# Kernel optimization log

Measured on AMD Instinct MI355X. Metric: run time of the kernel, lower is better.

Reference implementation:

```python
import jax, jax.numpy as jnp
import numpy as np

B, S, H = 32, 2048, 1024

def setup_inputs() -> dict:
    key = jax.random.key(0)
    ks = jax.random.split(key, 8)
    scale = 1.0 / np.sqrt(H)
    return {
        "query": jax.random.normal(ks[0], (B, H), jnp.float32),
        "keys": jax.random.normal(ks[1], (B, S, H), jnp.float32),
        "Wa_w": jax.random.uniform(ks[2], (H, H), jnp.float32, -scale, scale),
        "Wa_b": jax.random.uniform(ks[3], (H,), jnp.float32, -scale, scale),
        "Ua_w": jax.random.uniform(ks[4], (H, H), jnp.float32, -scale, scale),
        "Ua_b": jax.random.uniform(ks[5], (H,), jnp.float32, -scale, scale),
        "Va_w": jax.random.uniform(ks[6], (1, H), jnp.float32, -scale, scale),
        "Va_b": jax.random.uniform(ks[7], (1,), jnp.float32, -scale, scale),
    }

def reference(query, keys, Wa_w, Wa_b, Ua_w, Ua_b, Va_w, Va_b):
    # q_proj: [B, H]; k_proj: [B, S, H]  (torch Linear: x @ W^T + b)
    q_proj = query @ Wa_w.T + Wa_b
    k_proj = jnp.einsum("bsh,gh->bsg", keys, Ua_w) + Ua_b
    # scores: [B, S, 1] via thin Va projection of tanh-combined features
    scores = jnp.tanh(q_proj[:, None, :] + k_proj) @ Va_w.T + Va_b
    weights = jax.nn.softmax(scores, axis=1)            # [B, S, 1]
    context = jnp.einsum("bsx,bsh->bxh", weights, keys)  # [B, 1, H]
    return context, weights[:, :, 0]
```

## Files before the change

kernel.cpp:

```cpp
#include <hip/hip_runtime.h>
#include <hip/hip_bf16.h>
#include <stdint.h>

#define B_ 32
#define S_ 2048
#define H_ 1024

typedef __attribute__((ext_vector_type(8))) short short8;
typedef __attribute__((ext_vector_type(4))) float floatx4;

__device__ inline unsigned short f32_bf16(float f) {
    union { float f; unsigned u; } v; v.f = f;
    unsigned u = v.u;
    u += 0x7fff + ((u >> 16) & 1);
    return (unsigned short)(u >> 16);
}
__device__ inline unsigned pack_bf2(float a, float b) {
    return (unsigned)f32_bf16(a) | ((unsigned)f32_bf16(b) << 16);
}
__device__ inline float bf_lo(unsigned u) { union { unsigned u; float f; } v; v.u = u << 16; return v.f; }
__device__ inline float bf_hi(unsigned u) { union { unsigned u; float f; } v; v.u = u & 0xffff0000u; return v.f; }

__device__ inline float tanh_fast(float x) {
    float e = __expf(2.0f * x);
    return 1.0f - 2.0f / (e + 1.0f);
}

__device__ inline void gld16(const void* g, void* l) {
    __builtin_amdgcn_global_load_lds(
        (const __attribute__((address_space(1))) unsigned int*)g,
        (__attribute__((address_space(3))) unsigned int*)l, 16, 0, 0);
}

#define KCVT_BLOCKS 32768
#define UACVT_BLOCKS 512
#define ZS_BLOCKS 64
__global__ void k_prep(const float* __restrict__ keys, unsigned short* __restrict__ keysbf,
                       const float* __restrict__ ua, unsigned short* __restrict__ uab,
                       float* __restrict__ scores) {
    int blk = blockIdx.x, t = threadIdx.x;
    if (blk < KCVT_BLOCKS + UACVT_BLOCKS) {
        const float* src; unsigned short* dst; size_t base;
        if (blk < KCVT_BLOCKS) { src = keys; dst = keysbf; base = (size_t)blk * 2048; }
        else { src = ua; dst = uab; base = (size_t)(blk - KCVT_BLOCKS) * 2048; }
        float4 v0 = *(const float4*)(src + base + t * 4);
        float4 v1 = *(const float4*)(src + base + 1024 + t * 4);
        *(uint2*)(dst + base + t * 4)        = make_uint2(pack_bf2(v0.x, v0.y), pack_bf2(v0.z, v0.w));
        *(uint2*)(dst + base + 1024 + t * 4) = make_uint2(pack_bf2(v1.x, v1.y), pack_bf2(v1.z, v1.w));
    } else {
        int zb = blk - KCVT_BLOCKS - UACVT_BLOCKS;
        float4 z = {0.f, 0.f, 0.f, 0.f};
        *(float4*)(scores + zb * 1024 + t * 4) = z;
    }
}

__global__ void k_qproj(const float* __restrict__ query, const float* __restrict__ Wa_w,
                        const float* __restrict__ Wa_b, const float* __restrict__ Ua_b,
                        float* __restrict__ qsum) {
    __shared__ float qs_l[32][68];
    int g0 = blockIdx.x * 16;
    int t = threadIdx.x;
    int r = t >> 4;
    int l = t & 15;
    int g = g0 + r;
    float acc[32];
#pragma unroll
    for (int b = 0; b < 32; ++b) acc[b] = 0.0f;

    int sb = t >> 3;
    int sc = (t & 7) * 8;
    for (int hc = 0; hc < 16; ++hc) {
        __syncthreads();
        float4 v0 = *(const float4*)(query + (size_t)sb * H_ + hc * 64 + sc);
        float4 v1 = *(const float4*)(query + (size_t)sb * H_ + hc * 64 + sc + 4);
        *(float4*)&qs_l[sb][sc]     = v0;
        *(float4*)&qs_l[sb][sc + 4] = v1;
        __syncthreads();
        float4 w = *(const float4*)(Wa_w + (size_t)g * H_ + hc * 64 + l * 4);
#pragma unroll
        for (int b = 0; b < 32; ++b) {
            float4 q4 = *(const float4*)&qs_l[b][l * 4];
            acc[b] += w.x * q4.x + w.y * q4.y + w.z * q4.z + w.w * q4.w;
        }
    }
#pragma unroll
    for (int b = 0; b < 32; ++b) {
        float a = acc[b];
        a += __shfl_xor(a, 1); a += __shfl_xor(a, 2);
        a += __shfl_xor(a, 4); a += __shfl_xor(a, 8);
        acc[b] = a;
    }
    if (l == 0) {
        float bias = Wa_b[g] + Ua_b[g];
#pragma unroll
        for (int b = 0; b < 32; ++b) qsum[b * H_ + g] = acc[b] + bias;
    }
}

#define BM 128
#define BN 128
#define BK 32

__global__ __launch_bounds__(256, 3) void k_scores(
    const unsigned short* __restrict__ keysbf, const unsigned short* __restrict__ uab,
    const float* __restrict__ qsum, const float* __restrict__ va,
    float* __restrict__ scores)
{
    __shared__ unsigned short Al[BM * BK];
    __shared__ unsigned short Bl[BN * BK];

    int bx = blockIdx.x;
    int x  = bx & 7;
    int i  = bx >> 3;
    int tile_m = x * 64 + (i >> 3);
    int nc     = i & 7;
    int m_base = tile_m * BM;
    int b      = m_base >> 11;
    int g0     = nc * BN;

    int tid = threadIdx.x;
    int wid = tid >> 6, lane = tid & 63;
    int wm = wid >> 1, wn = wid & 1;
    int q = lane >> 4, cn = lane & 15;

    int rl = lane >> 2, cg = lane & 3;
    int rA0 = wid * 32 + rl,      rA1 = wid * 32 + 16 + rl;
    int gA0 = cg ^ ((rA0 >> 1) & 3), gA1 = cg ^ ((rA1 >> 1) & 3);
    const unsigned short* pA0 = keysbf + (size_t)(m_base + rA0) * H_ + gA0 * 8;
    const unsigned short* pA1 = keysbf + (size_t)(m_base + rA1) * H_ + gA1 * 8;
    const unsigned short* pB0 = uab + (size_t)(g0 + rA0) * H_ + gA0 * 8;
    const unsigned short* pB1 = uab + (size_t)(g0 + rA1) * H_ + gA1 * 8;
    unsigned short* lA0 = &Al[(wid * 32) * BK];
    unsigned short* lA1 = &Al[(wid * 32 + 16) * BK];
    unsigned short* lB0 = &Bl[(wid * 32) * BK];
    unsigned short* lB1 = &Bl[(wid * 32 + 16) * BK];

    int aoff[4], boff[4];
#pragma unroll
    for (int ii = 0; ii < 4; ++ii) {
        int r = wm * 64 + ii * 16 + cn;
        aoff[ii] = r * BK + (q ^ ((r >> 1) & 3)) * 8;
        int rb = wn * 64 + ii * 16 + cn;
        boff[ii] = rb * BK + (q ^ ((rb >> 1) & 3)) * 8;
    }

    floatx4 acc[4][4];
#pragma unroll
    for (int ii = 0; ii < 4; ++ii)
#pragma unroll
        for (int jj = 0; jj < 4; ++jj)
            acc[ii][jj] = (floatx4)(0.0f);

    for (int kc = 0; kc < H_ / BK; ++kc) {
        __syncthreads();
        int ko = kc * BK;
        gld16(pA0 + ko, lA0);
        gld16(pA1 + ko, lA1);
        gld16(pB0 + ko, lB0);
        gld16(pB1 + ko, lB1);
        __syncthreads();
        short8 af[4], bf[4];
#pragma unroll
        for (int ii = 0; ii < 4; ++ii) af[ii] = *(const short8*)&Al[aoff[ii]];
#pragma unroll
        for (int jj = 0; jj < 4; ++jj) bf[jj] = *(const short8*)&Bl[boff[jj]];
#pragma unroll
        for (int ii = 0; ii < 4; ++ii)
#pragma unroll
            for (int jj = 0; jj < 4; ++jj)
                acc[ii][jj] = __builtin_amdgcn_mfma_f32_16x16x32_bf16(
                    af[ii], bf[jj], acc[ii][jj], 0, 0, 0);
    }

    float qs[4], vw[4];
#pragma unroll
    for (int jj = 0; jj < 4; ++jj) {
        int g = g0 + wn * 64 + jj * 16 + cn;
        qs[jj] = qsum[b * H_ + g];
        vw[jj] = va[g];
    }
#pragma unroll
    for (int ii = 0; ii < 4; ++ii) {
        float rs[4] = {0.f, 0.f, 0.f, 0.f};
#pragma unroll
        for (int jj = 0; jj < 4; ++jj) {
#pragma unroll
            for (int r = 0; r < 4; ++r)
                rs[r] += vw[jj] * tanh_fast(qs[jj] + acc[ii][jj][r]);
        }
#pragma unroll
        for (int r = 0; r < 4; ++r) {
            for (int mm = 1; mm < 16; mm <<= 1)
                rs[r] += __shfl_xor(rs[r], mm);
        }
        if (cn == 0) {
            int msrow = m_base + wm * 64 + ii * 16 + q * 4;
            float* sp = scores + b * S_ + (msrow & (S_ - 1));
            atomicAdd(sp + 0, rs[0]);
            atomicAdd(sp + 1, rs[1]);
            atomicAdd(sp + 2, rs[2]);
            atomicAdd(sp + 3, rs[3]);
        }
    }
}

__global__ void k_softmax(const float* __restrict__ scores, float* __restrict__ weights) {
    int b = blockIdx.x;
    int t = threadIdx.x;
    __shared__ float red[4];
    float v[8];
    float mx = -1e30f;
#pragma unroll
    for (int k = 0; k < 8; ++k) { v[k] = scores[b * S_ + t + k * 256]; mx = fmaxf(mx, v[k]); }
    for (int mm = 1; mm < 64; mm <<= 1) mx = fmaxf(mx, __shfl_xor(mx, mm));
    if ((t & 63) == 0) red[t >> 6] = mx;
    __syncthreads();
    mx = fmaxf(fmaxf(red[0], red[1]), fmaxf(red[2], red[3]));
    float sum = 0.0f;
#pragma unroll
    for (int k = 0; k < 8; ++k) { v[k] = __expf(v[k] - mx); sum += v[k]; }
    for (int mm = 1; mm < 64; mm <<= 1) sum += __shfl_xor(sum, mm);
    __syncthreads();
    if ((t & 63) == 0) red[t >> 6] = sum;
    __syncthreads();
    sum = red[0] + red[1] + red[2] + red[3];
    float inv = 1.0f / sum;
#pragma unroll
    for (int k = 0; k < 8; ++k) weights[b * S_ + t + k * 256] = v[k] * inv;
}

__global__ void k_ctx1(const unsigned short* __restrict__ keysbf,
                       const float* __restrict__ weights, float* __restrict__ partial) {
    int blk = blockIdx.x;
    int b = blk >> 5, sc = blk & 31;
    int t = threadIdx.x;
    __shared__ float wl[64];
    if (t < 64) wl[t] = weights[b * S_ + sc * 64 + t];
    __syncthreads();
    const uint4* kp = (const uint4*)(keysbf + (size_t)(b * S_ + sc * 64) * H_);
    int col = t & 127;
    int rp  = t >> 7;
    float a0=0,a1=0,a2=0,a3=0,a4=0,a5=0,a6=0,a7=0;
#pragma unroll 8
    for (int s = rp; s < 64; s += 2) {
        uint4 v = kp[(size_t)s * 128 + col];
        float w = wl[s];
        a0 += w * bf_lo(v.x); a1 += w * bf_hi(v.x);
        a2 += w * bf_lo(v.y); a3 += w * bf_hi(v.y);
        a4 += w * bf_lo(v.z); a5 += w * bf_hi(v.z);
        a6 += w * bf_lo(v.w); a7 += w * bf_hi(v.w);
    }
    float* pp = partial + (size_t)(b * 64 + sc * 2 + rp) * H_ + col * 8;
    float4 o0 = {a0, a1, a2, a3}, o1 = {a4, a5, a6, a7};
    *(float4*)pp = o0;
    *(float4*)(pp + 4) = o1;
}

__global__ void k_ctx2(const float* __restrict__ partial, float* __restrict__ ctx) {
    int b = blockIdx.x;
    int t = threadIdx.x;
    float4 a = {0.f, 0.f, 0.f, 0.f};
#pragma unroll 8
    for (int j = 0; j < 64; ++j) {
        float4 p = *(const float4*)(partial + (size_t)(b * 64 + j) * H_ + t * 4);
        a.x += p.x; a.y += p.y; a.z += p.z; a.w += p.w;
    }
    *(float4*)(ctx + b * H_ + t * 4) = a;
}

extern "C" void kernel_launch(void* const* d_in, const int* in_sizes, int n_in,
                              void* d_out, int out_size, void* d_ws, size_t ws_size,
                              hipStream_t stream) {
    const float* query = (const float*)d_in[0];
    const float* keys  = (const float*)d_in[1];
    const float* Wa_w  = (const float*)d_in[2];
    const float* Wa_b  = (const float*)d_in[3];
    const float* Ua_w  = (const float*)d_in[4];
    const float* Ua_b  = (const float*)d_in[5];
    const float* Va_w  = (const float*)d_in[6];

    float* out     = (float*)d_out;
    float* ctx     = out;
    float* weights = out + B_ * H_;

    char* ws = (char*)d_ws;
    unsigned short* keysbf = (unsigned short*)ws;
    unsigned short* uab    = (unsigned short*)(ws + 134217728);
    float*          qsum   = (float*)(ws + 134217728 + 2097152);
    float*          scores = (float*)(ws + 134217728 + 2097152 + 131072);
    float*          partial= (float*)(ws + 134217728 + 2097152 + 131072 + 262144);

    k_prep   <<<KCVT_BLOCKS + UACVT_BLOCKS + ZS_BLOCKS, 256, 0, stream>>>(keys, keysbf, Ua_w, uab, scores);
    k_qproj  <<<64, 256, 0, stream>>>(query, Wa_w, Wa_b, Ua_b, qsum);
    k_scores <<<4096, 256, 0, stream>>>(keysbf, uab, qsum, Va_w, scores);
    k_softmax<<<B_, 256, 0, stream>>>(scores, weights);
    k_ctx1   <<<B_ * 32, 256, 0, stream>>>(keysbf, weights, partial);
    k_ctx2   <<<B_, 256, 0, stream>>>(partial, ctx);
}
```

Before: 627.7 us.

## Double GEMM K-tile to 64 with 8-way swizzle and fold qproj into prep kernel

The scores GEMM now stages a 64-wide K slice per iteration instead of 32, with a new XOR swizzle over 8 column groups and two MFMA sub-steps per tile. This halves the number of barrier-separated load/compute iterations and the synchronisation overhead. The query projection is merged into the prep kernel as extra blocks, removing one kernel launch and letting it overlap with the conversion work. LDS use per block doubles to 32KB, which may reduce occupancy at the requested 3 blocks per CU. The prep kernel also now carries the qproj shared array and register load.

```diff
diff --git a/kernel.cpp b/kernel.cpp
--- a/kernel.cpp
+++ b/kernel.cpp
@@ -35,9 +35,13 @@
 #define KCVT_BLOCKS 32768
 #define UACVT_BLOCKS 512
 #define ZS_BLOCKS 64
+#define QP_BLOCKS 64
 __global__ void k_prep(const float* __restrict__ keys, unsigned short* __restrict__ keysbf,
                        const float* __restrict__ ua, unsigned short* __restrict__ uab,
-                       float* __restrict__ scores) {
+                       float* __restrict__ scores,
+                       const float* __restrict__ query, const float* __restrict__ Wa_w,
+                       const float* __restrict__ Wa_b, const float* __restrict__ Ua_b,
+                       float* __restrict__ qsum) {
     int blk = blockIdx.x, t = threadIdx.x;
     if (blk < KCVT_BLOCKS + UACVT_BLOCKS) {
         const float* src; unsigned short* dst; size_t base;
@@ -47,59 +51,51 @@
         float4 v1 = *(const float4*)(src + base + 1024 + t * 4);
         *(uint2*)(dst + base + t * 4)        = make_uint2(pack_bf2(v0.x, v0.y), pack_bf2(v0.z, v0.w));
         *(uint2*)(dst + base + 1024 + t * 4) = make_uint2(pack_bf2(v1.x, v1.y), pack_bf2(v1.z, v1.w));
-    } else {
+    } else if (blk < KCVT_BLOCKS + UACVT_BLOCKS + ZS_BLOCKS) {
         int zb = blk - KCVT_BLOCKS - UACVT_BLOCKS;
         float4 z = {0.f, 0.f, 0.f, 0.f};
         *(float4*)(scores + zb * 1024 + t * 4) = z;
-    }
-}
-
-__global__ void k_qproj(const float* __restrict__ query, const float* __restrict__ Wa_w,
-                        const float* __restrict__ Wa_b, const float* __restrict__ Ua_b,
-                        float* __restrict__ qsum) {
-    __shared__ float qs_l[32][68];
-    int g0 = blockIdx.x * 16;
-    int t = threadIdx.x;
-    int r = t >> 4;
-    int l = t & 15;
-    int g = g0 + r;
-    float acc[32];
-#pragma unroll
-    for (int b = 0; b < 32; ++b) acc[b] = 0.0f;
-
-    int sb = t >> 3;
-    int sc = (t & 7) * 8;
-    for (int hc = 0; hc < 16; ++hc) {
-        __syncthreads();
-        float4 v0 = *(const float4*)(query + (size_t)sb * H_ + hc * 64 + sc);
-        float4 v1 = *(const float4*)(query + (size_t)sb * H_ + hc * 64 + sc + 4);
-        *(float4*)&qs_l[sb][sc]     = v0;
-        *(float4*)&qs_l[sb][sc + 4] = v1;
-        __syncthreads();
-        float4 w = *(const float4*)(Wa_w + (size_t)g * H_ + hc * 64 + l * 4);
+    } else {
+        __shared__ float qs_l[32][68];
+        int g0 = (blk - KCVT_BLOCKS - UACVT_BLOCKS - ZS_BLOCKS) * 16;
+        int r = t >> 4, l = t & 15;
+        int g = g0 + r;
+        float acc[32];
+#pragma unroll
+        for (int b = 0; b < 32; ++b) acc[b] = 0.0f;
+        int sb = t >> 3, sc = (t & 7) * 8;
+        for (int hc = 0; hc < 16; ++hc) {
+            __syncthreads();
+            float4 v0 = *(const float4*)(query + (size_t)sb * H_ + hc * 64 + sc);
+            float4 v1 = *(const float4*)(query + (size_t)sb * H_ + hc * 64 + sc + 4);
+            *(float4*)&qs_l[sb][sc]     = v0;
+            *(float4*)&qs_l[sb][sc + 4] = v1;
+            __syncthreads();
+            float4 w = *(const float4*)(Wa_w + (size_t)g * H_ + hc * 64 + l * 4);
+#pragma unroll
+            for (int b = 0; b < 32; ++b) {
+                float4 q4 = *(const float4*)&qs_l[b][l * 4];
+                acc[b] += w.x * q4.x + w.y * q4.y + w.z * q4.z + w.w * q4.w;
+            }
+        }
 #pragma unroll
         for (int b = 0; b < 32; ++b) {
-            float4 q4 = *(const float4*)&qs_l[b][l * 4];
-            acc[b] += w.x * q4.x + w.y * q4.y + w.z * q4.z + w.w * q4.w;
-        }
-    }
-#pragma unroll
-    for (int b = 0; b < 32; ++b) {
-        float a = acc[b];
-        a += __shfl_xor(a, 1); a += __shfl_xor(a, 2);
-        a += __shfl_xor(a, 4); a += __shfl_xor(a, 8);
-        acc[b] = a;
-    }
-    if (l == 0) {
-        float bias = Wa_b[g] + Ua_b[g];
-#pragma unroll
-        for (int b = 0; b < 32; ++b) qsum[b * H_ + g] = acc[b] + bias;
+            float a = acc[b];
+            a += __shfl_xor(a, 1); a += __shfl_xor(a, 2);
+            a += __shfl_xor(a, 4); a += __shfl_xor(a, 8);
+            acc[b] = a;
+        }
+        if (l == 0) {
+            float bias = Wa_b[g] + Ua_b[g];
+#pragma unroll
+            for (int b = 0; b < 32; ++b) qsum[b * H_ + g] = acc[b] + bias;
+        }
     }
 }
 
 #define BM 128
 #define BN 128
-#define BK 32
+#define BK 64
 
 __global__ __launch_bounds__(256, 3) void k_scores(
     const unsigned short* __restrict__ keysbf, const unsigned short* __restrict__ uab,
@@ -123,26 +119,31 @@
     int wm = wid >> 1, wn = wid & 1;
     int q = lane >> 4, cn = lane & 15;
 
-    int rl = lane >> 2, cg = lane & 3;
-    int rA0 = wid * 32 + rl,      rA1 = wid * 32 + 16 + rl;
-    int gA0 = cg ^ ((rA0 >> 1) & 3), gA1 = cg ^ ((rA1 >> 1) & 3);
-    const unsigned short* pA0 = keysbf + (size_t)(m_base + rA0) * H_ + gA0 * 8;
-    const unsigned short* pA1 = keysbf + (size_t)(m_base + rA1) * H_ + gA1 * 8;
-    const unsigned short* pB0 = uab + (size_t)(g0 + rA0) * H_ + gA0 * 8;
-    const unsigned short* pB1 = uab + (size_t)(g0 + rA1) * H_ + gA1 * 8;
-    unsigned short* lA0 = &Al[(wid * 32) * BK];
-    unsigned short* lA1 = &Al[(wid * 32 + 16) * BK];
-    unsigned short* lB0 = &Bl[(wid * 32) * BK];
-    unsigned short* lB1 = &Bl[(wid * 32 + 16) * BK];
-
-    int aoff[4], boff[4];
-#pragma unroll
-    for (int ii = 0; ii < 4; ++ii) {
-        int r = wm * 64 + ii * 16 + cn;
-        aoff[ii] = r * BK + (q ^ ((r >> 1) & 3)) * 8;
-        int rb = wn * 64 + ii * 16 + cn;
-        boff[ii] = rb * BK + (q ^ ((rb >> 1) & 3)) * 8;
-    }
+    int rl8 = lane >> 3;
+    int gcg = (lane & 7) ^ rl8;
+    const unsigned short* pA[4];
+    const unsigned short* pB[4];
+    unsigned short* lA[4];
+    unsigned short* lB[4];
+#pragma unroll
+    for (int j = 0; j < 4; ++j) {
+        int row = wid * 32 + j * 8 + rl8;
+        pA[j] = keysbf + (size_t)(m_base + row) * H_ + gcg * 8;
+        pB[j] = uab    + (size_t)(g0     + row) * H_ + gcg * 8;
+        lA[j] = &Al[(wid * 32 + j * 8) * BK];
+        lB[j] = &Bl[(wid * 32 + j * 8) * BK];
+    }
+
+    int aoff[2][4], boff[2][4];
+#pragma unroll
+    for (int kk = 0; kk < 2; ++kk)
+#pragma unroll
+        for (int ii = 0; ii < 4; ++ii) {
+            int r  = wm * 64 + ii * 16 + cn;
+            aoff[kk][ii] = r * BK + ((kk * 4 + q) ^ (r & 7)) * 8;
+            int rb = wn * 64 + ii * 16 + cn;
+            boff[kk][ii] = rb * BK + ((kk * 4 + q) ^ (rb & 7)) * 8;
+        }
 
     floatx4 acc[4][4];
 #pragma unroll
@@ -154,22 +155,26 @@
     for (int kc = 0; kc < H_ / BK; ++kc) {
         __syncthreads();
         int ko = kc * BK;
-        gld16(pA0 + ko, lA0);
-        gld16(pA1 + ko, lA1);
-        gld16(pB0 + ko, lB0);
-        gld16(pB1 + ko, lB1);
+#pragma unroll
+        for (int j = 0; j < 4; ++j) {
+            gld16(pA[j] + ko, lA[j]);
+            gld16(pB[j] + ko, lB[j]);
+        }
         __syncthreads();
-        short8 af[4], bf[4];
-#pragma unroll
-        for (int ii = 0; ii < 4; ++ii) af[ii] = *(const short8*)&Al[aoff[ii]];
-#pragma unroll
-        for (int jj = 0; jj < 4; ++jj) bf[jj] = *(const short8*)&Bl[boff[jj]];
-#pragma unroll
-        for (int ii = 0; ii < 4; ++ii)
-#pragma unroll
-            for (int jj = 0; jj < 4; ++jj)
-                acc[ii][jj] = __builtin_amdgcn_mfma_f32_16x16x32_bf16(
-                    af[ii], bf[jj], acc[ii][jj], 0, 0, 0);
+#pragma unroll
+        for (int kk = 0; kk < 2; ++kk) {
+            short8 af[4], bf[4];
+#pragma unroll
+            for (int ii = 0; ii < 4; ++ii) af[ii] = *(const short8*)&Al[aoff[kk][ii]];
+#pragma unroll
+            for (int jj = 0; jj < 4; ++jj) bf[jj] = *(const short8*)&Bl[boff[kk][jj]];
+#pragma unroll
+            for (int ii = 0; ii < 4; ++ii)
+#pragma unroll
+                for (int jj = 0; jj < 4; ++jj)
+                    acc[ii][jj] = __builtin_amdgcn_mfma_f32_16x16x32_bf16(
+                        af[ii], bf[jj], acc[ii][jj], 0, 0, 0);
+        }
     }
 
     float qs[4], vw[4];
@@ -290,8 +295,8 @@
     float*          scores = (float*)(ws + 134217728 + 2097152 + 131072);
     float*          partial= (float*)(ws + 134217728 + 2097152 + 131072 + 262144);
 
-    k_prep   <<<KCVT_BLOCKS + UACVT_BLOCKS + ZS_BLOCKS, 256, 0, stream>>>(keys, keysbf, Ua_w, uab, scores);
-    k_qproj  <<<64, 256, 0, stream>>>(query, Wa_w, Wa_b, Ua_b, qsum);
+    k_prep   <<<KCVT_BLOCKS + UACVT_BLOCKS + ZS_BLOCKS + QP_BLOCKS, 256, 0, stream>>>(
+        keys, keysbf, Ua_w, uab, scores, query, Wa_w, Wa_b, Ua_b, qsum);
     k_scores <<<4096, 256, 0, stream>>>(keysbf, uab, qsum, Va_w, scores);
     k_softmax<<<B_, 256, 0, stream>>>(scores, weights);
     k_ctx1   <<<B_ * 32, 256, 0, stream>>>(keysbf, weights, partial);
```

Measured after the change: 600.2 us. 4.4% less time.
